# Kernel optimization log

Measured on AMD Instinct MI355X. Metric: run time of the kernel, lower is better.

## Reference

```python
import jax, jax.numpy as jnp
import numpy as np
import math

EMBED_DIM = 1024
NUM_HEADS = 16
B, T = 4, 2048
HEAD_DIM = EMBED_DIM // NUM_HEADS


def setup_inputs() -> dict:
    key = jax.random.key(0)
    ks = jax.random.split(key, 9)
    s = 1.0 / math.sqrt(EMBED_DIM)
    x = jax.random.normal(ks[0], (B, T, EMBED_DIM), dtype=jnp.float32)
    # causal mask, broadcastable over (B, H)
    mask = jnp.tril(jnp.ones((T, T), dtype=bool))[None, None, :, :]
    Wq = jax.random.normal(ks[1], (EMBED_DIM, EMBED_DIM), dtype=jnp.float32) * s
    bq = jnp.zeros((EMBED_DIM,), dtype=jnp.float32)
    Wk = jax.random.normal(ks[2], (EMBED_DIM, EMBED_DIM), dtype=jnp.float32) * s
    bk = jnp.zeros((EMBED_DIM,), dtype=jnp.float32)
    Wv = jax.random.normal(ks[3], (EMBED_DIM, EMBED_DIM), dtype=jnp.float32) * s
    bv = jnp.zeros((EMBED_DIM,), dtype=jnp.float32)
    Wo = jax.random.normal(ks[4], (EMBED_DIM, EMBED_DIM), dtype=jnp.float32) * s
    bo = jnp.zeros((EMBED_DIM,), dtype=jnp.float32)
    return {"x": x, "mask": mask, "Wq": Wq, "bq": bq, "Wk": Wk, "bk": bk,
            "Wv": Wv, "bv": bv, "Wo": Wo, "bo": bo}


def reference(x, mask, Wq, bq, Wk, bk, Wv, bv, Wo, bo):
    Bsz, Tlen, C = x.shape
    H, D = NUM_HEADS, HEAD_DIM
    q = (x @ Wq + bq).reshape(Bsz, Tlen, H, D).transpose(0, 2, 1, 3)  # [B,H,T,D]
    k = (x @ Wk + bk).reshape(Bsz, Tlen, H, D).transpose(0, 2, 1, 3)
    v = (x @ Wv + bv).reshape(Bsz, Tlen, H, D).transpose(0, 2, 1, 3)
    scores = jnp.einsum('bhtd,bhsd->bhts', q, k) / math.sqrt(D)  # [B,H,T,T]
    scores = jnp.where(mask, scores, jnp.float32(-1e9))
    attn = jax.nn.softmax(scores, axis=-1)
    out = jnp.einsum('bhts,bhsd->bhtd', attn, v)  # [B,H,T,D]
    out = out.transpose(0, 2, 1, 3).reshape(Bsz, Tlen, C)
    return out @ Wo + bo
```

## Files before the change

kernel.cpp:

```cpp
#include <hip/hip_runtime.h>

#define SEQ   2048
#define NH    16
#define HD    64
#define EMB   1024
#define NB    4
#define MTOT  (NB*SEQ)
#define NT    (SEQ/64)

typedef _Float16 f16;
typedef _Float16 f16x4 __attribute__((ext_vector_type(4)));
typedef _Float16 f16x8 __attribute__((ext_vector_type(8)));
typedef float    f32x4 __attribute__((ext_vector_type(4)));

#define MFMA_F16(a,b,c) __builtin_amdgcn_mfma_f32_16x16x32_f16(a,b,c,0,0,0)

#define QSCALE 0.18033688011112043f

__device__ __forceinline__ void gload16(const f16* g, f16* l) {
  __builtin_amdgcn_global_load_lds(
      (const __attribute__((address_space(1))) void*)g,
      (__attribute__((address_space(3))) void*)l, 16, 0, 0);
}

__global__ __launch_bounds__(256) void cast_x_kernel(
    const float* __restrict__ x, f16* __restrict__ xh) {
  size_t i = ((size_t)blockIdx.x * 256 + threadIdx.x) * 8;
  float4 a = *(const float4*)(x + i);
  float4 b = *(const float4*)(x + i + 4);
  f16x8 o;
  o[0]=(f16)a.x; o[1]=(f16)a.y; o[2]=(f16)a.z; o[3]=(f16)a.w;
  o[4]=(f16)b.x; o[5]=(f16)b.y; o[6]=(f16)b.z; o[7]=(f16)b.w;
  *(f16x8*)(xh + i) = o;
}

__global__ __launch_bounds__(256) void wtrans_kernel(
    const float* __restrict__ W0, const float* __restrict__ W1,
    const float* __restrict__ W2, const float* __restrict__ W3,
    f16* __restrict__ O0, f16* __restrict__ O1,
    f16* __restrict__ O2, f16* __restrict__ O3) {
  const int z = blockIdx.z;
  const float* W = (z==0)?W0:(z==1)?W1:(z==2)?W2:W3;
  f16* O        = (z==0)?O0:(z==1)?O1:(z==2)?O2:O3;
  __shared__ float Tl[64][68];
  const int t = threadIdx.x;
  const int k0 = blockIdx.x * 64, n0 = blockIdx.y * 64;
  {
    const int r = t >> 2, c0 = (t & 3) * 16;
    const float* src = W + (size_t)(k0 + r) * EMB + n0 + c0;
    #pragma unroll
    for (int j = 0; j < 4; ++j) {
      float4 v = *(const float4*)(src + 4 * j);
      Tl[c0+4*j+0][r]=v.x; Tl[c0+4*j+1][r]=v.y;
      Tl[c0+4*j+2][r]=v.z; Tl[c0+4*j+3][r]=v.w;
    }
  }
  __syncthreads();
  {
    const int n = t >> 2, c0 = (t & 3) * 16;
    f16* dst = O + (size_t)(n0 + n) * EMB + k0 + c0;
    #pragma unroll
    for (int j = 0; j < 2; ++j) {
      f16x8 o;
      #pragma unroll
      for (int u = 0; u < 8; ++u) o[u] = (f16)Tl[n][c0 + 8*j + u];
      *(f16x8*)(dst + 8 * j) = o;
    }
  }
}

template<int MODE>
__device__ __forceinline__ void gemm_core(
    const f16* __restrict__ A, const f16* __restrict__ Bt,
    const float* __restrict__ bias, void* __restrict__ out,
    int m0, int n0, float scale) {
  __shared__ f16 As[128 * 64];
  __shared__ f16 Bs[128 * 64];
  const int tid  = threadIdx.x;
  const int lane = tid & 63, w = tid >> 6;
  const int g = lane >> 4, lx = lane & 15;
  const int wr = w >> 1, wc = w & 1;
  const int sr = lane >> 3, sc = lane & 7;

  f32x4 acc[4][4];
  const f32x4 z4 = {0.f, 0.f, 0.f, 0.f};
  #pragma unroll
  for (int i = 0; i < 4; ++i)
    #pragma unroll
    for (int j = 0; j < 4; ++j) acc[i][j] = z4;

  for (int k0 = 0; k0 < EMB; k0 += 64) {
    __syncthreads();
    #pragma unroll
    for (int ci = 0; ci < 4; ++ci) {
      const int i = 4 * w + ci;
      const int r = i * 8 + sr;
      const int c = sc ^ (r & 7);
      gload16(A  + (size_t)(m0 + r) * EMB + k0 + c * 8, &As[i * 512]);
      gload16(Bt + (size_t)(n0 + r) * EMB + k0 + c * 8, &Bs[i * 512]);
    }
    __syncthreads();

    #pragma unroll
    for (int h = 0; h < 2; ++h) {
      f16x8 af[4], bf[4];
      #pragma unroll
      for (int mf = 0; mf < 4; ++mf) {
        const int row = wr * 64 + mf * 16 + lx;
        const int off = (row * 128 + h * 64 + g * 16) ^ ((row & 7) << 4);
        af[mf] = *(const f16x8*)((const char*)As + off);
      }
      #pragma unroll
      for (int nf = 0; nf < 4; ++nf) {
        const int row = wc * 64 + nf * 16 + lx;
        const int off = (row * 128 + h * 64 + g * 16) ^ ((row & 7) << 4);
        bf[nf] = *(const f16x8*)((const char*)Bs + off);
      }
      #pragma unroll
      for (int mf = 0; mf < 4; ++mf)
        #pragma unroll
        for (int nf = 0; nf < 4; ++nf)
          acc[mf][nf] = MFMA_F16(af[mf], bf[nf], acc[mf][nf]);
    }
  }

  #pragma unroll
  for (int mf = 0; mf < 4; ++mf) {
    #pragma unroll
    for (int nf = 0; nf < 4; ++nf) {
      const int n  = n0 + wc * 64 + nf * 16 + lx;
      const int mb = m0 + wr * 64 + mf * 16 + g * 4;
      const float bv = bias[n];
      if (MODE == 2) {
        float* op = (float*)out;
        #pragma unroll
        for (int r = 0; r < 4; ++r)
          op[(size_t)(mb + r) * EMB + n] = acc[mf][nf][r] + bv;
      } else {
        const int b = mb >> 11, tt = mb & (SEQ - 1);
        const int hh = n >> 6, d = n & (HD - 1);
        f16* op = (f16*)out;
        if (MODE == 0) {
          #pragma unroll
          for (int r = 0; r < 4; ++r)
            op[((size_t)(b * NH + hh) * SEQ + tt + r) * HD + d] =
                (f16)((acc[mf][nf][r] + bv) * scale);
        } else {
          f16x4 o;
          #pragma unroll
          for (int r = 0; r < 4; ++r) o[r] = (f16)(acc[mf][nf][r] + bv);
          *(f16x4*)(op + ((size_t)(b * NH + hh) * HD + d) * SEQ + tt) = o;
        }
      }
    }
  }
}

__global__ __launch_bounds__(256) void qk_gemm_kernel(
    const f16* __restrict__ xh, const f16* __restrict__ wqt,
    const f16* __restrict__ wkt, const float* __restrict__ bq,
    const float* __restrict__ bk, f16* __restrict__ qh, f16* __restrict__ kh) {
  const int z = blockIdx.z;
  gemm_core<0>(xh, z ? wkt : wqt, z ? bk : bq, z ? kh : qh,
               blockIdx.x * 128, blockIdx.y * 128, z ? 1.0f : QSCALE);
}

__global__ __launch_bounds__(256) void v_gemm_kernel(
    const f16* __restrict__ xh, const f16* __restrict__ wvt,
    const float* __restrict__ bv, f16* __restrict__ vth) {
  gemm_core<1>(xh, wvt, bv, vth, blockIdx.x * 128, blockIdx.y * 128, 1.0f);
}

__global__ __launch_bounds__(256) void proj_gemm_kernel(
    const f16* __restrict__ ath, const f16* __restrict__ wot,
    const float* __restrict__ bo, float* __restrict__ out) {
  gemm_core<2>(ath, wot, bo, out, blockIdx.x * 128, blockIdx.y * 128, 1.0f);
}

__global__ __launch_bounds__(256, 4) void attn_kernel(
    const f16* __restrict__ Qh, const f16* __restrict__ Kh,
    const f16* __restrict__ Vth, f16* __restrict__ Att) {
  __shared__ f16 Ks[64 * 64];
  __shared__ f16 Vs[64 * 64];
  __shared__ f16 Ps[4][16 * 64];
  const int tid  = threadIdx.x;
  const int lane = tid & 63, w = tid >> 6;
  const int g = lane >> 4, lx = lane & 15;
  const int sr = lane >> 3, sc = lane & 7;
  const int p  = blockIdx.x;
  const int bh = blockIdx.y;
  const int qlo = p, qhi = NT - 1 - p;
  const int nkt = qhi + 1;
  const f16* qp = Qh  + (size_t)bh * SEQ * HD;
  const f16* kp = Kh  + (size_t)bh * SEQ * HD;
  const f16* vp = Vth + (size_t)bh * HD * SEQ;
  const int row0[2] = {qlo * 64 + w * 16, qhi * 64 + w * 16};

  f16x8 qf[2][2];
  #pragma unroll
  for (int part = 0; part < 2; ++part) {
    const int qrow = row0[part] + lx;
    #pragma unroll
    for (int h = 0; h < 2; ++h)
      qf[part][h] = *(const f16x8*)(qp + (size_t)qrow * HD + h * 32 + g * 8);
  }

  const f32x4 z4 = {0.f, 0.f, 0.f, 0.f};
  f32x4 oa[2][4];
  float m_i[2] = {-1e30f, -1e30f}, l_i[2] = {0.f, 0.f};
  #pragma unroll
  for (int part = 0; part < 2; ++part)
    #pragma unroll
    for (int df = 0; df < 4; ++df) oa[part][df] = z4;

  for (int kt = 0; kt < nkt; ++kt) {
    __syncthreads();
    #pragma unroll
    for (int ci = 0; ci < 2; ++ci) {
      const int i = 2 * w + ci;
      const int r = i * 8 + sr;
      const int c = sc ^ (r & 7);
      gload16(kp + (size_t)(kt * 64 + r) * HD + c * 8, &Ks[i * 512]);
      gload16(vp + (size_t)r * SEQ + kt * 64 + c * 8,  &Vs[i * 512]);
    }
    __syncthreads();

    const int npart = (kt <= qlo) ? 2 : 1;
    #pragma unroll
    for (int pi = 0; pi < 2; ++pi) {
      if (pi >= npart) continue;
      const int part = 1 - pi;
      const int qrow = row0[part] + lx;
      const bool diag = (kt == (part ? qhi : qlo));

      f32x4 sa[4];
      #pragma unroll
      for (int sf = 0; sf < 4; ++sf) sa[sf] = z4;
      __builtin_amdgcn_s_setprio(1);
      #pragma unroll
      for (int h = 0; h < 2; ++h)
        #pragma unroll
        for (int sf = 0; sf < 4; ++sf) {
          const int row = sf * 16 + lx;
          const int off = (row * 128 + h * 64 + g * 16) ^ ((row & 7) << 4);
          f16x8 kf = *(const f16x8*)((const char*)Ks + off);
          sa[sf] = MFMA_F16(kf, qf[part][h], sa[sf]);
        }
      __builtin_amdgcn_s_setprio(0);

      float rmax = -1e30f;
      #pragma unroll
      for (int sf = 0; sf < 4; ++sf)
        #pragma unroll
        for (int r = 0; r < 4; ++r) {
          float vsc = sa[sf][r];
          if (diag) {
            const int kv = kt * 64 + sf * 16 + g * 4 + r;
            if (kv > qrow) vsc = -1e30f;
          }
          sa[sf][r] = vsc;
          rmax = fmaxf(rmax, vsc);
        }
      rmax = fmaxf(rmax, __shfl_xor(rmax, 16));
      rmax = fmaxf(rmax, __shfl_xor(rmax, 32));
      const float mnew = fmaxf(m_i[part], rmax);
      const float corr = exp2f(m_i[part] - mnew);
      m_i[part] = mnew;
      float rsum = 0.f;
      #pragma unroll
      for (int sf = 0; sf < 4; ++sf)
        #pragma unroll
        for (int r = 0; r < 4; ++r) {
          const float pv = exp2f(sa[sf][r] - mnew);
          sa[sf][r] = pv;
          rsum += pv;
        }
      rsum += __shfl_xor(rsum, 16);
      rsum += __shfl_xor(rsum, 32);
      l_i[part] = l_i[part] * corr + rsum;

      #pragma unroll
      for (int sf = 0; sf < 4; ++sf) {
        f16x4 p4;
        #pragma unroll
        for (int r = 0; r < 4; ++r) p4[r] = (f16)sa[sf][r];
        const int off = (lx * 128 + sf * 32 + g * 8) ^ ((lx & 7) << 4);
        *(f16x4*)((char*)Ps[w] + off) = p4;
      }

      #pragma unroll
      for (int r = 0; r < 4; ++r) {
        const float cr = __shfl(corr, g * 4 + r, 64);
        #pragma unroll
        for (int df = 0; df < 4; ++df) oa[part][df][r] *= cr;
      }

      __builtin_amdgcn_s_setprio(1);
      #pragma unroll
      for (int hk = 0; hk < 2; ++hk) {
        const int offp = (lx * 128 + hk * 64 + g * 16) ^ ((lx & 7) << 4);
        f16x8 pf = *(const f16x8*)((const char*)Ps[w] + offp);
        #pragma unroll
        for (int df = 0; df < 4; ++df) {
          const int row = df * 16 + lx;
          const int offv = (row * 128 + hk * 64 + g * 16) ^ ((row & 7) << 4);
          f16x8 vf = *(const f16x8*)((const char*)Vs + offv);
          oa[part][df] = MFMA_F16(pf, vf, oa[part][df]);
        }
      }
      __builtin_amdgcn_s_setprio(0);
    }
  }

  const int b = bh >> 4, hh = bh & 15;
  #pragma unroll
  for (int part = 0; part < 2; ++part) {
    const float inv = 1.f / l_i[part];
    #pragma unroll
    for (int r = 0; r < 4; ++r) {
      const float ir = __shfl(inv, g * 4 + r, 64);
      const int t = row0[part] + g * 4 + r;
      f16* dst = Att + ((size_t)b * SEQ + t) * EMB + hh * HD;
      #pragma unroll
      for (int df = 0; df < 4; ++df)
        dst[df * 16 + lx] = (f16)(oa[part][df][r] * ir);
    }
  }
}

extern "C" void kernel_launch(void* const* d_in, const int* in_sizes, int n_in,
                              void* d_out, int out_size, void* d_ws, size_t ws_size,
                              hipStream_t stream) {
  (void)in_sizes; (void)n_in; (void)out_size; (void)ws_size;
  const float* x  = (const float*)d_in[0];
  const float* Wq = (const float*)d_in[2];
  const float* bq = (const float*)d_in[3];
  const float* Wk = (const float*)d_in[4];
  const float* bk = (const float*)d_in[5];
  const float* Wv = (const float*)d_in[6];
  const float* bv = (const float*)d_in[7];
  const float* Wo = (const float*)d_in[8];
  const float* bo = (const float*)d_in[9];

  f16* xh  = (f16*)d_ws;
  f16* wqt = xh  + (size_t)MTOT * EMB;
  f16* wkt = wqt + (size_t)EMB * EMB;
  f16* wvt = wkt + (size_t)EMB * EMB;
  f16* wot = wvt + (size_t)EMB * EMB;
  f16* qh  = wot + (size_t)EMB * EMB;
  f16* kh  = qh  + (size_t)MTOT * EMB;
  f16* vth = kh  + (size_t)MTOT * EMB;
  f16* ath = vth + (size_t)MTOT * EMB;

  cast_x_kernel<<<dim3(MTOT * EMB / (256 * 8)), 256, 0, stream>>>(x, xh);
  wtrans_kernel<<<dim3(16, 16, 4), 256, 0, stream>>>(
      Wq, Wk, Wv, Wo, wqt, wkt, wvt, wot);
  qk_gemm_kernel<<<dim3(MTOT / 128, EMB / 128, 2), 256, 0, stream>>>(
      xh, wqt, wkt, bq, bk, qh, kh);
  v_gemm_kernel<<<dim3(MTOT / 128, EMB / 128), 256, 0, stream>>>(
      xh, wvt, bv, vth);
  attn_kernel<<<dim3(NT / 2, NB * NH), 256, 0, stream>>>(qh, kh, vth, ath);
  proj_gemm_kernel<<<dim3(MTOT / 128, EMB / 128), 256, 0, stream>>>(
      ath, wot, bo, (float*)d_out);
}
```

Measured before the change: 198.6 us.

## Double-buffer K/V tiles, share K fragments across parts, lazily rescale softmax

Attention K/V tiles now live in two LDS buffers. The next tile's global-to-LDS load is issued right after the barrier, so it overlaps with compute on the current tile and one barrier per iteration is removed. When both query parts are active, each K fragment is read from LDS once and feeds both QK^T MFMA chains. Online-softmax rescaling of the accumulators and row sum is skipped unless some row max exceeds the running max by more than 8 (log2 units), which removes shuffles and multiplies in the common case. The cost is doubled K/V LDS, which could limit occupancy, and unnormalized P values up to 2^8 stored in fp16.

```diff
diff --git a/kernel.cpp b/kernel.cpp
--- a/kernel.cpp
+++ b/kernel.cpp
@@ -180,8 +180,8 @@
 __global__ __launch_bounds__(256, 4) void attn_kernel(
     const f16* __restrict__ Qh, const f16* __restrict__ Kh,
     const f16* __restrict__ Vth, f16* __restrict__ Att) {
-  __shared__ f16 Ks[64 * 64];
-  __shared__ f16 Vs[64 * 64];
+  __shared__ f16 Ks[2][64 * 64];
+  __shared__ f16 Vs[2][64 * 64];
   __shared__ f16 Ps[4][16 * 64];
   const int tid  = threadIdx.x;
   const int lane = tid & 63, w = tid >> 6;
@@ -213,41 +213,29 @@
     #pragma unroll
     for (int df = 0; df < 4; ++df) oa[part][df] = z4;
 
-  for (int kt = 0; kt < nkt; ++kt) {
-    __syncthreads();
+  auto stage = [&](int kt_, int b_) {
     #pragma unroll
     for (int ci = 0; ci < 2; ++ci) {
       const int i = 2 * w + ci;
       const int r = i * 8 + sr;
       const int c = sc ^ (r & 7);
-      gload16(kp + (size_t)(kt * 64 + r) * HD + c * 8, &Ks[i * 512]);
-      gload16(vp + (size_t)r * SEQ + kt * 64 + c * 8,  &Vs[i * 512]);
-    }
+      gload16(kp + (size_t)(kt_ * 64 + r) * HD + c * 8, &Ks[b_][i * 512]);
+      gload16(vp + (size_t)r * SEQ + kt_ * 64 + c * 8,  &Vs[b_][i * 512]);
+    }
+  };
+
+  stage(0, 0);
+
+  for (int kt = 0; kt < nkt; ++kt) {
+    const int buf = kt & 1;
     __syncthreads();
-
-    const int npart = (kt <= qlo) ? 2 : 1;
-    #pragma unroll
-    for (int pi = 0; pi < 2; ++pi) {
-      if (pi >= npart) continue;
-      const int part = 1 - pi;
+    if (kt + 1 < nkt) stage(kt + 1, buf ^ 1);
+
+    const f16* ksb = Ks[buf];
+    const f16* vsb = Vs[buf];
+
+    auto do_part = [&](int part, f32x4* sa, bool diag) {
       const int qrow = row0[part] + lx;
-      const bool diag = (kt == (part ? qhi : qlo));
-
-      f32x4 sa[4];
-      #pragma unroll
-      for (int sf = 0; sf < 4; ++sf) sa[sf] = z4;
-      __builtin_amdgcn_s_setprio(1);
-      #pragma unroll
-      for (int h = 0; h < 2; ++h)
-        #pragma unroll
-        for (int sf = 0; sf < 4; ++sf) {
-          const int row = sf * 16 + lx;
-          const int off = (row * 128 + h * 64 + g * 16) ^ ((row & 7) << 4);
-          f16x8 kf = *(const f16x8*)((const char*)Ks + off);
-          sa[sf] = MFMA_F16(kf, qf[part][h], sa[sf]);
-        }
-      __builtin_amdgcn_s_setprio(0);
-
       float rmax = -1e30f;
       #pragma unroll
       for (int sf = 0; sf < 4; ++sf)
@@ -257,27 +245,37 @@
           if (diag) {
             const int kv = kt * 64 + sf * 16 + g * 4 + r;
             if (kv > qrow) vsc = -1e30f;
+            sa[sf][r] = vsc;
           }
-          sa[sf][r] = vsc;
           rmax = fmaxf(rmax, vsc);
         }
       rmax = fmaxf(rmax, __shfl_xor(rmax, 16));
       rmax = fmaxf(rmax, __shfl_xor(rmax, 32));
-      const float mnew = fmaxf(m_i[part], rmax);
-      const float corr = exp2f(m_i[part] - mnew);
-      m_i[part] = mnew;
+      if (!__all(rmax <= m_i[part] + 8.f)) {
+        const float mnew = fmaxf(m_i[part], rmax);
+        const float corr = exp2f(m_i[part] - mnew);
+        m_i[part] = mnew;
+        l_i[part] *= corr;
+        #pragma unroll
+        for (int r = 0; r < 4; ++r) {
+          const float cr = __shfl(corr, g * 4 + r, 64);
+          #pragma unroll
+          for (int df = 0; df < 4; ++df) oa[part][df][r] *= cr;
+        }
+      }
+      const float mcur = m_i[part];
       float rsum = 0.f;
       #pragma unroll
       for (int sf = 0; sf < 4; ++sf)
         #pragma unroll
         for (int r = 0; r < 4; ++r) {
-          const float pv = exp2f(sa[sf][r] - mnew);
+          const float pv = exp2f(sa[sf][r] - mcur);
           sa[sf][r] = pv;
           rsum += pv;
         }
       rsum += __shfl_xor(rsum, 16);
       rsum += __shfl_xor(rsum, 32);
-      l_i[part] = l_i[part] * corr + rsum;
+      l_i[part] += rsum;
 
       #pragma unroll
       for (int sf = 0; sf < 4; ++sf) {
@@ -288,13 +286,6 @@
         *(f16x4*)((char*)Ps[w] + off) = p4;
       }
 
-      #pragma unroll
-      for (int r = 0; r < 4; ++r) {
-        const float cr = __shfl(corr, g * 4 + r, 64);
-        #pragma unroll
-        for (int df = 0; df < 4; ++df) oa[part][df][r] *= cr;
-      }
-
       __builtin_amdgcn_s_setprio(1);
       #pragma unroll
       for (int hk = 0; hk < 2; ++hk) {
@@ -304,11 +295,47 @@
         for (int df = 0; df < 4; ++df) {
           const int row = df * 16 + lx;
           const int offv = (row * 128 + hk * 64 + g * 16) ^ ((row & 7) << 4);
-          f16x8 vf = *(const f16x8*)((const char*)Vs + offv);
+          f16x8 vf = *(const f16x8*)((const char*)vsb + offv);
           oa[part][df] = MFMA_F16(pf, vf, oa[part][df]);
         }
       }
       __builtin_amdgcn_s_setprio(0);
+    };
+
+    if (kt <= qlo) {
+      f32x4 s0[4], s1[4];
+      #pragma unroll
+      for (int sf = 0; sf < 4; ++sf) { s0[sf] = z4; s1[sf] = z4; }
+      __builtin_amdgcn_s_setprio(1);
+      #pragma unroll
+      for (int h = 0; h < 2; ++h)
+        #pragma unroll
+        for (int sf = 0; sf < 4; ++sf) {
+          const int row = sf * 16 + lx;
+          const int off = (row * 128 + h * 64 + g * 16) ^ ((row & 7) << 4);
+          f16x8 kf = *(const f16x8*)((const char*)ksb + off);
+          s0[sf] = MFMA_F16(kf, qf[0][h], s0[sf]);
+          s1[sf] = MFMA_F16(kf, qf[1][h], s1[sf]);
+        }
+      __builtin_amdgcn_s_setprio(0);
+      do_part(1, s1, false);
+      do_part(0, s0, kt == qlo);
+    } else {
+      f32x4 s1[4];
+      #pragma unroll
+      for (int sf = 0; sf < 4; ++sf) s1[sf] = z4;
+      __builtin_amdgcn_s_setprio(1);
+      #pragma unroll
+      for (int h = 0; h < 2; ++h)
+        #pragma unroll
+        for (int sf = 0; sf < 4; ++sf) {
+          const int row = sf * 16 + lx;
+          const int off = (row * 128 + h * 64 + g * 16) ^ ((row & 7) << 4);
+          f16x8 kf = *(const f16x8*)((const char*)ksb + off);
+          s1[sf] = MFMA_F16(kf, qf[1][h], s1[sf]);
+        }
+      __builtin_amdgcn_s_setprio(0);
+      do_part(1, s1, kt == qhi);
     }
   }
 
```

Measured after the change: 348.4 us. 1.75x slower.
